# Kernel optimization log

Hardware: AMD Instinct MI355X
Metric: run time of the kernel (lower is better)

Reference implementation:

```python
import jax, jax.numpy as jnp
import numpy as np

B, S, E, C = 128, 256, 768, 4


def setup_inputs() -> dict:
    key = jax.random.key(0)
    ks = jax.random.split(key, 8)
    questions = jax.random.normal(ks[0], (B, E), dtype=jnp.float32)
    segments = jax.random.normal(ks[1], (B, S, E), dtype=jnp.float32)
    W1 = jax.random.normal(ks[2], (2 * E, E), dtype=jnp.float32) * 0.02
    b1 = jnp.zeros((E,), dtype=jnp.float32)
    W2 = jax.random.normal(ks[3], (E, E // 2), dtype=jnp.float32) * 0.02
    b2 = jnp.zeros((E // 2,), dtype=jnp.float32)
    W3 = jax.random.normal(ks[4], (E // 2, C), dtype=jnp.float32) * 0.02
    b3 = jnp.zeros((C,), dtype=jnp.float32)
    num_segments = jax.random.randint(ks[5], (B,), 1, S + 1, dtype=jnp.int32)
    return {"questions": questions, "segments": segments, "W1": W1, "b1": b1,
            "W2": W2, "b2": b2, "W3": W3, "b3": b3, "num_segments": num_segments}


def reference(questions, segments, W1, b1, W2, b2, W3, b3, num_segments):
    # --- MLP instance scores (call()): concat question emb with every segment emb ---
    q = jnp.broadcast_to(questions[:, None, :], segments.shape)      # [B,S,E]
    x = jnp.concatenate([q, segments], axis=-1)                      # [B,S,2E]
    h = jax.nn.gelu(x @ W1 + b1, approximate=False)                  # keras gelu is exact
    h = jax.nn.gelu(h @ W2 + b2, approximate=False)
    preds = jax.nn.softmax(h @ W3 + b3, axis=-1)                     # [B,S,C]

    # --- per-bag noisy-OR style aggregation (aggregate_loss inner math, vectorized) ---
    # In the TF code, for class cid: s_j = sum(preds[j,:cid]) (exclusive cumsum over
    # classes), and product_of_sum_prob ACCUMULATES across the i loop, so
    # update_i = preds[i,cid] * cumprod_i( prod_{j!=k} s_j ) (leave-one-out products).
    mask = jnp.arange(S)[None, :] < num_segments[:, None]            # [B,S]
    mC = mask[..., None]                                             # [B,S,1]
    s = jnp.cumsum(preds, axis=-1) - preds                           # exclusive cumsum, [B,S,C]
    s_m = jnp.where(mC, s, 1.0)                                      # padded -> multiplicative identity
    # leave-one-out product over the segment axis via prefix/suffix cumprods
    cp_f = jnp.cumprod(s_m, axis=1)
    prefix = jnp.concatenate([jnp.ones_like(s_m[:, :1]), cp_f[:, :-1]], axis=1)
    cp_b = jnp.cumprod(s_m[:, ::-1], axis=1)[:, ::-1]
    suffix = jnp.concatenate([cp_b[:, 1:], jnp.ones_like(s_m[:, :1])], axis=1)
    L = prefix * suffix                                              # prod_{j!=k} s_j, [B,S,C]
    cpL = jnp.cumprod(L, axis=1)                                     # running product over i (padding is at the end)
    sum_term = jnp.sum(jnp.where(mC, preds * cpL, 0.0), axis=1)      # [B,C]
    prod_term = jnp.prod(jnp.where(mC, preds, 1.0), axis=1)          # prod_i preds[i,cid]
    agg = sum_term / jnp.float32(C) + prod_term                      # bag_pred_agg_scores, [B,C]
    return agg
```

## Files before the change

kernel.cpp:

```cpp
#include <hip/hip_runtime.h>
#include <hip/hip_bf16.h>


typedef __attribute__((ext_vector_type(8))) short short8;
typedef __attribute__((ext_vector_type(8))) unsigned short ushort8;
typedef __attribute__((ext_vector_type(16))) float f32x16;
typedef __attribute__((ext_vector_type(8))) int i32x8;
typedef __attribute__((ext_vector_type(4))) int i32x4;

__device__ __forceinline__ unsigned short f2bf(float f) {
    union { float f; unsigned int u; } c; c.f = f;
    unsigned int u = c.u;
    unsigned int r = (u + 0x7FFFu + ((u >> 16) & 1u)) >> 16;
    return (unsigned short)r;
}
__device__ __forceinline__ float bf2f(unsigned short u) {
    union { unsigned int u; float f; } c; c.u = ((unsigned int)u) << 16;
    return c.f;
}
__device__ __forceinline__ float gelu_fast(float x) {
    float x2 = x * x;
    float y2 = 1.5957691216057308f * (x + 0.044715f * x2 * x);
    float e = __expf(y2);
    float t = 1.0f - 2.0f * __builtin_amdgcn_rcpf(e + 1.0f);
    return 0.5f * x * (1.0f + t);
}

typedef const __attribute__((address_space(1))) void* gas_t;
typedef __attribute__((address_space(3))) void* las_t;
__device__ __forceinline__ void g2l16(const void* g, void* l) {
    __builtin_amdgcn_global_load_lds((gas_t)g, (las_t)l, 16, 0, 0);
}

__device__ __forceinline__ unsigned int f4_to_fp8x4(float a, float b, float c, float d) {
    int lo = __builtin_amdgcn_cvt_pk_fp8_f32(a, b, 0, 0);
    return (unsigned int)__builtin_amdgcn_cvt_pk_fp8_f32(c, d, lo, 1);
}
__device__ __forceinline__ unsigned char f_to_fp8(float a) {
    return (unsigned char)(__builtin_amdgcn_cvt_pk_fp8_f32(a, a, 0, 0) & 0xFF);
}

#define PREP_Q    96
#define PREP_TR1E 240
#define PREP_TR2E 312
#define PREP_END  12600

__global__ __launch_bounds__(256) void prep_kernel(
    const float* __restrict__ segments, unsigned char* __restrict__ segF8,
    const float* __restrict__ W1, unsigned char* __restrict__ W1t8,
    const float* __restrict__ W2, unsigned char* __restrict__ W2t8,
    const float* __restrict__ questions, float* __restrict__ qW1p)
{
    __shared__ __align__(16) char sh[16640];
    const int bid = blockIdx.x, tid = threadIdx.x;

    if (bid < PREP_Q) {
        const int s = bid / 24, rem = bid % 24;
        const int n0 = (rem % 12) * 64, m0 = (rem / 12) * 64;
        float (*As)[64] = (float(*)[64])sh;
        float (*Bs)[64] = (float(*)[64])(sh + 4096);
        const int tn = tid & 15, tm = tid >> 4;
        float acc[4][4] = {};
        const int la_m = tid >> 2;
        const int la_k = (tid & 3) << 2;
        const int lb_k = tid >> 4;
        const int lb_n = (tid & 15) << 2;
        const float* Aptr = questions + (size_t)(m0 + la_m) * 768 + la_k;
        const float* Bptr = W1 + (size_t)lb_k * 768 + n0 + lb_n;
        const int kbeg = s * 192, kend = kbeg + 192;
        for (int k0 = kbeg; k0 < kend; k0 += 16) {
            float4 av = *(const float4*)(Aptr + k0);
            float4 bv = *(const float4*)(Bptr + (size_t)k0 * 768);
            As[la_k + 0][la_m] = av.x;
            As[la_k + 1][la_m] = av.y;
            As[la_k + 2][la_m] = av.z;
            As[la_k + 3][la_m] = av.w;
            *(float4*)&Bs[lb_k][lb_n] = bv;
            __syncthreads();
            #pragma unroll
            for (int k = 0; k < 16; k++) {
                float4 a = *(const float4*)&As[k][tm << 2];
                float4 b = *(const float4*)&Bs[k][tn << 2];
                float ar[4] = {a.x, a.y, a.z, a.w};
                float br[4] = {b.x, b.y, b.z, b.w};
                #pragma unroll
                for (int i = 0; i < 4; i++)
                    #pragma unroll
                    for (int j = 0; j < 4; j++)
                        acc[i][j] += ar[i] * br[j];
            }
            __syncthreads();
        }
        float* outp = qW1p + (size_t)s * 128 * 768;
        #pragma unroll
        for (int i = 0; i < 4; i++) {
            int row = m0 + (tm << 2) + i;
            int colBase = n0 + (tn << 2);
            *(float4*)&outp[(size_t)row * 768 + colBase] =
                make_float4(acc[i][0], acc[i][1], acc[i][2], acc[i][3]);
        }
        return;
    }

    if (bid < PREP_TR2E) {
        const float* in; unsigned char* outp; int R, C, bx, by;
        if (bid < PREP_TR1E) {
            int idx = bid - PREP_Q; bx = idx % 12; by = idx / 12;
            in = W1 + 768 * 768; outp = W1t8; R = 768; C = 768;
        } else {
            int idx = bid - PREP_TR1E; bx = idx % 6; by = idx / 6;
            in = W2; outp = W2t8; R = 768; C = 384;
        }
        float (*t)[65] = (float(*)[65])sh;
        int r0 = by * 64, c0 = bx * 64;
        int tx = tid & 63, ty = tid >> 6;
        #pragma unroll
        for (int p = 0; p < 16; p++) {
            int row = ty * 16 + p;
            t[row][tx] = in[(size_t)(r0 + row) * C + c0 + tx];
        }
        __syncthreads();
        #pragma unroll
        for (int p = 0; p < 16; p++) {
            int orow = ty * 16 + p;
            outp[(size_t)(c0 + orow) * R + r0 + tx] = f_to_fp8(t[tx][orow]);
        }
        return;
    }

    {
        long i = (long)(bid - PREP_TR2E) * 256 + tid;
        const float4* in = (const float4*)segments;
        float4 a = in[2 * i], b = in[2 * i + 1];
        unsigned int lo = f4_to_fp8x4(a.x, a.y, a.z, a.w);
        unsigned int hi = f4_to_fp8x4(b.x, b.y, b.z, b.w);
        *(uint2*)(segF8 + i * 8) = make_uint2(lo, hi);
    }
}

template<int MODE>
__global__ __launch_bounds__(256) void mfma_gemm_f8(
    const unsigned char* __restrict__ A8,
    const unsigned char* __restrict__ Bt8,
    const float* __restrict__ bias,
    const float* __restrict__ rowAdd,
    void* __restrict__ CoutV,
    int M, int N, int K,
    const float* __restrict__ W3p)
{
    __shared__ __align__(16) unsigned char smem8[32768 + (MODE == 2 ? 2048 : 0)];
    unsigned char* As = smem8;
    unsigned char* Bs = smem8 + 8192;
    const int tid = threadIdx.x;
    const int wave = tid >> 6, lane = tid & 63;
    const int m0 = blockIdx.y * 128, n0 = blockIdx.x * 128;
    const int wm = (wave & 1) * 64, wn = (wave >> 1) * 64;

    if constexpr (MODE == 2) {
        if (tid < 128)
            ((float4*)(smem8 + 32768))[tid] = ((const float4*)W3p)[n0 + tid];
    }

    f32x16 acc[2][2] = {};

    const int srow = tid >> 2;
    const int schunk = (tid & 3) ^ ((srow >> 1) & 3);
    const unsigned char* Ag = A8 + (size_t)(m0 + srow) * K + schunk * 16;
    const unsigned char* Bg = Bt8 + (size_t)(n0 + srow) * K + schunk * 16;
    unsigned char* Al = As + tid * 16;
    unsigned char* Bl = Bs + tid * 16;

    const int fm = lane & 31, fq = lane >> 5;

    for (int k0 = 0; k0 < K; k0 += 64) {
        g2l16(Ag + k0, Al);
        g2l16(Ag + (size_t)64 * K + k0, Al + 4096);
        g2l16(Bg + k0, Bl);
        g2l16(Bg + (size_t)64 * K + k0, Bl + 4096);
        __syncthreads();

        i32x8 av[2], bv[2];
        #pragma unroll
        for (int i = 0; i < 2; i++) {
            int rw = wm + i * 32 + fm, key = (rw >> 1) & 3;
            i32x4 lo = *(const i32x4*)&As[rw * 64 + (((fq << 1) | 0) ^ key) * 16];
            i32x4 hi = *(const i32x4*)&As[rw * 64 + (((fq << 1) | 1) ^ key) * 16];
            av[i][0] = lo[0]; av[i][1] = lo[1]; av[i][2] = lo[2]; av[i][3] = lo[3];
            av[i][4] = hi[0]; av[i][5] = hi[1]; av[i][6] = hi[2]; av[i][7] = hi[3];
        }
        #pragma unroll
        for (int j = 0; j < 2; j++) {
            int rw = wn + j * 32 + fm, key = (rw >> 1) & 3;
            i32x4 lo = *(const i32x4*)&Bs[rw * 64 + (((fq << 1) | 0) ^ key) * 16];
            i32x4 hi = *(const i32x4*)&Bs[rw * 64 + (((fq << 1) | 1) ^ key) * 16];
            bv[j][0] = lo[0]; bv[j][1] = lo[1]; bv[j][2] = lo[2]; bv[j][3] = lo[3];
            bv[j][4] = hi[0]; bv[j][5] = hi[1]; bv[j][6] = hi[2]; bv[j][7] = hi[3];
        }
        #pragma unroll
        for (int i = 0; i < 2; i++)
            #pragma unroll
            for (int j = 0; j < 2; j++)
                acc[i][j] = __builtin_amdgcn_mfma_scale_f32_32x32x64_f8f6f4(
                    av[i], bv[j], acc[i][j], 0, 0,
                    0, 127, 0, 127);
        __syncthreads();
    }

    #pragma unroll
    for (int j = 0; j < 2; j++) {
        int coll = wn + j * 32 + fm;
        int col = n0 + coll;
        float add = bias[col];
        if (rowAdd) {
            const float* radd = rowAdd + (size_t)(m0 >> 8) * N;
            add += radd[col] + radd[col + 98304] +
                   radd[col + 2 * 98304] + radd[col + 3 * 98304];
        }
        #pragma unroll
        for (int i = 0; i < 2; i++) {
            int rbase = wm + i * 32 + 4 * fq;
            #pragma unroll
            for (int reg = 0; reg < 16; reg++) {
                int rowl = rbase + (reg & 3) + 8 * (reg >> 2);
                float v = gelu_fast(acc[i][j][reg] + add);
                if constexpr (MODE == 1) smem8[rowl * 128 + coll] = f_to_fp8(v);
                else ((unsigned short*)smem8)[rowl * 128 + coll] = f2bf(v);
            }
        }
    }
    __syncthreads();
    if constexpr (MODE == 1) {
        unsigned char* Cout = (unsigned char*)CoutV;
        #pragma unroll
        for (int it = 0; it < 4; it++) {
            int idx = it * 256 + tid;
            int r = idx >> 3, cc = (idx & 7) * 16;
            *(uint4*)&Cout[(size_t)(m0 + r) * N + n0 + cc] =
                *(const uint4*)&smem8[r * 128 + cc];
        }
    } else if constexpr (MODE == 2) {
        const float4* w3sh = (const float4*)(smem8 + 32768);
        const unsigned short* tile = (const unsigned short*)smem8;
        int r = tid >> 1, ch = tid & 1;
        const unsigned short* rowp = tile + r * 128 + ch * 64;
        float4 a = make_float4(0.f, 0.f, 0.f, 0.f);
        #pragma unroll
        for (int k = 0; k < 8; k++) {
            int kk = k ^ (r & 7);
            ushort8 u = *(const ushort8*)(rowp + kk * 8);
            #pragma unroll
            for (int jj = 0; jj < 8; jj++) {
                float h = bf2f(u[jj]);
                float4 wv2 = w3sh[ch * 64 + kk * 8 + jj];
                a.x += h * wv2.x; a.y += h * wv2.y;
                a.z += h * wv2.z; a.w += h * wv2.w;
            }
        }
        a.x += __shfl_xor(a.x, 1); a.y += __shfl_xor(a.y, 1);
        a.z += __shfl_xor(a.z, 1); a.w += __shfl_xor(a.w, 1);
        if (ch == 0)
            ((float4*)CoutV)[(size_t)blockIdx.x * 32768 + m0 + r] = a;
    } else {
        unsigned short* Cout = (unsigned short*)CoutV;
        #pragma unroll
        for (int it = 0; it < 8; it++) {
            int idx = it * 256 + tid;
            int r = idx >> 4, cc = (idx & 15) * 8;
            *(ushort8*)&Cout[(size_t)(m0 + r) * N + n0 + cc] =
                *(const ushort8*)&((unsigned short*)smem8)[r * 128 + cc];
        }
    }
}

__device__ __forceinline__ float4 f4mul(float4 a, float4 b) {
    return make_float4(a.x * b.x, a.y * b.y, a.z * b.z, a.w * b.w);
}

__device__ __forceinline__ float4 block_scan_prod(float4 v, int lane, int wv,
                                                  float4* wtot) {
    #pragma unroll
    for (int off = 1; off < 64; off <<= 1) {
        float4 t;
        t.x = __shfl_up(v.x, off); t.y = __shfl_up(v.y, off);
        t.z = __shfl_up(v.z, off); t.w = __shfl_up(v.w, off);
        if (lane >= off) v = f4mul(v, t);
    }
    if (lane == 63) wtot[wv] = v;
    __syncthreads();
    float4 pre = make_float4(1.f, 1.f, 1.f, 1.f);
    #pragma unroll
    for (int w = 0; w < 3; w++)
        if (w < wv) pre = f4mul(pre, wtot[w]);
    __syncthreads();
    return f4mul(pre, v);
}

__global__ __launch_bounds__(256) void head_kernel(
    const float* __restrict__ pp,
    const float* __restrict__ b3,
    const int* __restrict__ nseg,
    float* __restrict__ out)
{
    __shared__ float4 xbuf[256];
    __shared__ float4 wtot[4];
    const int b = blockIdx.x, tid = threadIdx.x;
    const int lane = tid & 63, wv = tid >> 6;
    const float4 ones = make_float4(1.f, 1.f, 1.f, 1.f);

    const float4* ppv = (const float4*)pp;
    size_t row = (size_t)b * 256 + tid;
    float4 a0 = ppv[row], a1 = ppv[row + 32768], a2 = ppv[row + 65536];
    float4 acc = make_float4(a0.x + a1.x + a2.x + b3[0],
                             a0.y + a1.y + a2.y + b3[1],
                             a0.z + a1.z + a2.z + b3[2],
                             a0.w + a1.w + a2.w + b3[3]);
    float m = fmaxf(fmaxf(acc.x, acc.y), fmaxf(acc.z, acc.w));
    float e0 = __expf(acc.x - m), e1 = __expf(acc.y - m),
          e2 = __expf(acc.z - m), e3 = __expf(acc.w - m);
    float inv = 1.0f / (e0 + e1 + e2 + e3);
    float4 p = make_float4(e0 * inv, e1 * inv, e2 * inv, e3 * inv);

    const int n = nseg[b];
    bool msk = tid < n;
    float s1 = p.x, s2 = s1 + p.y, s3 = s2 + p.z;
    float4 sm = msk ? make_float4(0.f, s1, s2, s3) : ones;

    float4 isc = block_scan_prod(sm, lane, wv, wtot);
    xbuf[tid] = isc;
    __syncthreads();
    float4 pfx = (tid > 0) ? xbuf[tid - 1] : ones;
    __syncthreads();

    xbuf[255 - tid] = sm;
    __syncthreads();
    float4 rsm = xbuf[tid];
    __syncthreads();
    float4 risc = block_scan_prod(rsm, lane, wv, wtot);
    xbuf[tid] = risc;
    __syncthreads();
    float4 sfx = (tid < 255) ? xbuf[254 - tid] : ones;
    __syncthreads();

    float4 L = f4mul(pfx, sfx);
    float4 cpL = block_scan_prod(L, lane, wv, wtot);

    float4 term = msk ? f4mul(p, cpL) : make_float4(0.f, 0.f, 0.f, 0.f);
    float4 pm = msk ? p : ones;
    #pragma unroll
    for (int off = 32; off > 0; off >>= 1) {
        term.x += __shfl_xor(term.x, off); term.y += __shfl_xor(term.y, off);
        term.z += __shfl_xor(term.z, off); term.w += __shfl_xor(term.w, off);
        pm.x *= __shfl_xor(pm.x, off); pm.y *= __shfl_xor(pm.y, off);
        pm.z *= __shfl_xor(pm.z, off); pm.w *= __shfl_xor(pm.w, off);
    }
    if (lane == 0) { xbuf[wv] = term; xbuf[4 + wv] = pm; }
    __syncthreads();
    if (tid == 0) {
        float4 st = make_float4(0.f, 0.f, 0.f, 0.f);
        float4 pr = ones;
        #pragma unroll
        for (int w = 0; w < 4; w++) {
            float4 t = xbuf[w], q = xbuf[4 + w];
            st.x += t.x; st.y += t.y; st.z += t.z; st.w += t.w;
            pr = f4mul(pr, q);
        }
        ((float4*)out)[b] = make_float4(0.25f * st.x + pr.x,
                                        0.25f * st.y + pr.y,
                                        0.25f * st.z + pr.z,
                                        0.25f * st.w + pr.w);
    }
}

extern "C" void kernel_launch(void* const* d_in, const int* in_sizes, int n_in,
                              void* d_out, int out_size, void* d_ws, size_t ws_size,
                              hipStream_t stream) {
    (void)in_sizes; (void)n_in; (void)out_size; (void)ws_size;
    const float* questions = (const float*)d_in[0];
    const float* segments  = (const float*)d_in[1];
    const float* W1 = (const float*)d_in[2];
    const float* b1 = (const float*)d_in[3];
    const float* W2 = (const float*)d_in[4];
    const float* b2 = (const float*)d_in[5];
    const float* W3 = (const float*)d_in[6];
    const float* b3 = (const float*)d_in[7];
    const int*  nseg = (const int*)d_in[8];
    float* out = (float*)d_out;

    char* w = (char*)d_ws;
    float* qW1p = (float*)w;                   w += (size_t)4 * 128 * 768 * 4;
    unsigned char*  W1t8 = (unsigned char*)w;  w += (size_t)768 * 768;
    unsigned char*  W2t8 = (unsigned char*)w;  w += (size_t)384 * 768;
    unsigned char*  segF8 = (unsigned char*)w; w += (size_t)32768 * 768;
    unsigned char*  H1f8 = (unsigned char*)w;  w += (size_t)32768 * 768;
    float* ppreds = (float*)w;                 w += (size_t)3 * 32768 * 4 * 4;

    prep_kernel<<<PREP_END, 256, 0, stream>>>(
        segments, segF8, W1, W1t8, W2, W2t8, questions, qW1p);
    mfma_gemm_f8<1><<<dim3(6, 256), 256, 0, stream>>>(
        segF8, W1t8, b1, qW1p, H1f8, 32768, 768, 768, nullptr);
    mfma_gemm_f8<2><<<dim3(3, 256), 256, 0, stream>>>(
        H1f8, W2t8, b2, nullptr, ppreds, 32768, 384, 768, W3);
    head_kernel<<<128, 256, 0, stream>>>(ppreds, b3, nseg, out);
}
```

Before: 243.9 us.

## Double-buffer GEMM K loop, swizzle block order, and split question projection kernel

The fp8 MFMA GEMM now double-buffers its LDS tiles, issuing the next K-slab's global-to-LDS loads before computing on the current one, and drops one barrier per iteration. Block indices are remapped in an XCD-aware swizzle so neighbouring tiles share L2. The question×W1 projection moves into its own kernel that uses 8 K-splits with larger per-thread tiles and no per-step syncs, and the GEMM epilogue sums 8 partials instead of 4. The aim is to hide load latency and improve cache locality, at the cost of an extra kernel launch and more partial-sum reads.

```diff
diff --git a/kernel.cpp b/kernel.cpp
--- a/kernel.cpp
+++ b/kernel.cpp
@@ -40,75 +40,73 @@
     return (unsigned char)(__builtin_amdgcn_cvt_pk_fp8_f32(a, a, 0, 0) & 0xFF);
 }
 
-#define PREP_Q    96
-#define PREP_TR1E 240
-#define PREP_TR2E 312
-#define PREP_END  12600
-
-__global__ __launch_bounds__(256) void prep_kernel(
+__global__ __launch_bounds__(256) void prep_q_kernel(
+    const float* __restrict__ questions, const float* __restrict__ W1,
+    float* __restrict__ qW1p)
+{
+    __shared__ __align__(16) float As[96][132];
+    __shared__ __align__(16) float Bs[96][64];
+    const int tid = threadIdx.x;
+    const int nt = blockIdx.x % 12, sp = blockIdx.x / 12;
+    const int n0 = nt * 64, kbeg = sp * 96;
+
+    for (int i = tid; i < 3072; i += 256) {
+        int row = i / 24, c4 = i % 24;
+        float4 v = ((const float4*)questions)[row * 192 + (kbeg >> 2) + c4];
+        int kb = c4 * 4;
+        As[kb + 0][row] = v.x; As[kb + 1][row] = v.y;
+        As[kb + 2][row] = v.z; As[kb + 3][row] = v.w;
+    }
+    for (int i = tid; i < 1536; i += 256) {
+        int row = i / 16, c4 = i % 16;
+        float4 v = ((const float4*)W1)[(size_t)(kbeg + row) * 192 + (n0 >> 2) + c4];
+        *(float4*)&Bs[row][c4 * 4] = v;
+    }
+    __syncthreads();
+
+    const int tm = tid >> 4, tn = tid & 15;
+    float acc[8][4] = {};
+    #pragma unroll 2
+    for (int k = 0; k < 96; k++) {
+        float4 a0 = *(const float4*)&As[k][tm * 8];
+        float4 a1 = *(const float4*)&As[k][tm * 8 + 4];
+        float4 b  = *(const float4*)&Bs[k][tn * 4];
+        float ar[8] = {a0.x, a0.y, a0.z, a0.w, a1.x, a1.y, a1.z, a1.w};
+        float br[4] = {b.x, b.y, b.z, b.w};
+        #pragma unroll
+        for (int i = 0; i < 8; i++)
+            #pragma unroll
+            for (int j = 0; j < 4; j++)
+                acc[i][j] += ar[i] * br[j];
+    }
+    float* outp = qW1p + (size_t)sp * 128 * 768;
+    #pragma unroll
+    for (int i = 0; i < 8; i++) {
+        int row = tm * 8 + i;
+        *(float4*)&outp[(size_t)row * 768 + n0 + tn * 4] =
+            make_float4(acc[i][0], acc[i][1], acc[i][2], acc[i][3]);
+    }
+}
+
+#define PR_TR1E 144
+#define PR_TR2E 216
+#define PR_END  12504
+
+__global__ __launch_bounds__(256) void prep_rest_kernel(
     const float* __restrict__ segments, unsigned char* __restrict__ segF8,
     const float* __restrict__ W1, unsigned char* __restrict__ W1t8,
-    const float* __restrict__ W2, unsigned char* __restrict__ W2t8,
-    const float* __restrict__ questions, float* __restrict__ qW1p)
+    const float* __restrict__ W2, unsigned char* __restrict__ W2t8)
 {
     __shared__ __align__(16) char sh[16640];
     const int bid = blockIdx.x, tid = threadIdx.x;
 
-    if (bid < PREP_Q) {
-        const int s = bid / 24, rem = bid % 24;
-        const int n0 = (rem % 12) * 64, m0 = (rem / 12) * 64;
-        float (*As)[64] = (float(*)[64])sh;
-        float (*Bs)[64] = (float(*)[64])(sh + 4096);
-        const int tn = tid & 15, tm = tid >> 4;
-        float acc[4][4] = {};
-        const int la_m = tid >> 2;
-        const int la_k = (tid & 3) << 2;
-        const int lb_k = tid >> 4;
-        const int lb_n = (tid & 15) << 2;
-        const float* Aptr = questions + (size_t)(m0 + la_m) * 768 + la_k;
-        const float* Bptr = W1 + (size_t)lb_k * 768 + n0 + lb_n;
-        const int kbeg = s * 192, kend = kbeg + 192;
-        for (int k0 = kbeg; k0 < kend; k0 += 16) {
-            float4 av = *(const float4*)(Aptr + k0);
-            float4 bv = *(const float4*)(Bptr + (size_t)k0 * 768);
-            As[la_k + 0][la_m] = av.x;
-            As[la_k + 1][la_m] = av.y;
-            As[la_k + 2][la_m] = av.z;
-            As[la_k + 3][la_m] = av.w;
-            *(float4*)&Bs[lb_k][lb_n] = bv;
-            __syncthreads();
-            #pragma unroll
-            for (int k = 0; k < 16; k++) {
-                float4 a = *(const float4*)&As[k][tm << 2];
-                float4 b = *(const float4*)&Bs[k][tn << 2];
-                float ar[4] = {a.x, a.y, a.z, a.w};
-                float br[4] = {b.x, b.y, b.z, b.w};
-                #pragma unroll
-                for (int i = 0; i < 4; i++)
-                    #pragma unroll
-                    for (int j = 0; j < 4; j++)
-                        acc[i][j] += ar[i] * br[j];
-            }
-            __syncthreads();
-        }
-        float* outp = qW1p + (size_t)s * 128 * 768;
-        #pragma unroll
-        for (int i = 0; i < 4; i++) {
-            int row = m0 + (tm << 2) + i;
-            int colBase = n0 + (tn << 2);
-            *(float4*)&outp[(size_t)row * 768 + colBase] =
-                make_float4(acc[i][0], acc[i][1], acc[i][2], acc[i][3]);
-        }
-        return;
-    }
-
-    if (bid < PREP_TR2E) {
+    if (bid < PR_TR2E) {
         const float* in; unsigned char* outp; int R, C, bx, by;
-        if (bid < PREP_TR1E) {
-            int idx = bid - PREP_Q; bx = idx % 12; by = idx / 12;
+        if (bid < PR_TR1E) {
+            int idx = bid; bx = idx % 12; by = idx / 12;
             in = W1 + 768 * 768; outp = W1t8; R = 768; C = 768;
         } else {
-            int idx = bid - PREP_TR1E; bx = idx % 6; by = idx / 6;
+            int idx = bid - PR_TR1E; bx = idx % 6; by = idx / 6;
             in = W2; outp = W2t8; R = 768; C = 384;
         }
         float (*t)[65] = (float(*)[65])sh;
@@ -129,7 +127,7 @@
     }
 
     {
-        long i = (long)(bid - PREP_TR2E) * 256 + tid;
+        long i = (long)(bid - PR_TR2E) * 256 + tid;
         const float4* in = (const float4*)segments;
         float4 a = in[2 * i], b = in[2 * i + 1];
         unsigned int lo = f4_to_fp8x4(a.x, a.y, a.z, a.w);
@@ -149,11 +147,14 @@
     const float* __restrict__ W3p)
 {
     __shared__ __align__(16) unsigned char smem8[32768 + (MODE == 2 ? 2048 : 0)];
-    unsigned char* As = smem8;
-    unsigned char* Bs = smem8 + 8192;
     const int tid = threadIdx.x;
     const int wave = tid >> 6, lane = tid & 63;
-    const int m0 = blockIdx.y * 128, n0 = blockIdx.x * 128;
+
+    const int nwg = gridDim.x * gridDim.y;
+    const int bidl = blockIdx.y * gridDim.x + blockIdx.x;
+    const int cpx = nwg >> 3;
+    const int swz = (bidl & 7) * cpx + (bidl >> 3);
+    const int m0 = (swz / gridDim.x) * 128, n0 = (swz % gridDim.x) * 128;
     const int wm = (wave & 1) * 64, wn = (wave >> 1) * 64;
 
     if constexpr (MODE == 2) {
@@ -167,18 +168,25 @@
     const int schunk = (tid & 3) ^ ((srow >> 1) & 3);
     const unsigned char* Ag = A8 + (size_t)(m0 + srow) * K + schunk * 16;
     const unsigned char* Bg = Bt8 + (size_t)(n0 + srow) * K + schunk * 16;
-    unsigned char* Al = As + tid * 16;
-    unsigned char* Bl = Bs + tid * 16;
 
     const int fm = lane & 31, fq = lane >> 5;
 
+#define STAGE_K(buf, kk) do {                                   \
+        unsigned char* _d = smem8 + (buf) * 16384 + tid * 16;   \
+        g2l16(Ag + (kk), _d);                                   \
+        g2l16(Ag + (size_t)64 * K + (kk), _d + 4096);           \
+        g2l16(Bg + (kk), _d + 8192);                            \
+        g2l16(Bg + (size_t)64 * K + (kk), _d + 12288);          \
+    } while (0)
+
+    STAGE_K(0, 0);
+    __syncthreads();
+    int cur = 0;
     for (int k0 = 0; k0 < K; k0 += 64) {
-        g2l16(Ag + k0, Al);
-        g2l16(Ag + (size_t)64 * K + k0, Al + 4096);
-        g2l16(Bg + k0, Bl);
-        g2l16(Bg + (size_t)64 * K + k0, Bl + 4096);
-        __syncthreads();
-
+        if (k0 + 64 < K) STAGE_K(cur ^ 1, k0 + 64);
+
+        const unsigned char* As = smem8 + cur * 16384;
+        const unsigned char* Bs = As + 8192;
         i32x8 av[2], bv[2];
         #pragma unroll
         for (int i = 0; i < 2; i++) {
@@ -204,7 +212,9 @@
                     av[i], bv[j], acc[i][j], 0, 0,
                     0, 127, 0, 127);
         __syncthreads();
-    }
+        cur ^= 1;
+    }
+#undef STAGE_K
 
     #pragma unroll
     for (int j = 0; j < 2; j++) {
@@ -212,9 +222,9 @@
         int col = n0 + coll;
         float add = bias[col];
         if (rowAdd) {
-            const float* radd = rowAdd + (size_t)(m0 >> 8) * N;
-            add += radd[col] + radd[col + 98304] +
-                   radd[col + 2 * 98304] + radd[col + 3 * 98304];
+            const float* radd = rowAdd + (size_t)(m0 >> 8) * N + col;
+            #pragma unroll
+            for (int s = 0; s < 8; s++) add += radd[(size_t)s * 98304];
         }
         #pragma unroll
         for (int i = 0; i < 2; i++) {
@@ -259,16 +269,7 @@
         a.x += __shfl_xor(a.x, 1); a.y += __shfl_xor(a.y, 1);
         a.z += __shfl_xor(a.z, 1); a.w += __shfl_xor(a.w, 1);
         if (ch == 0)
-            ((float4*)CoutV)[(size_t)blockIdx.x * 32768 + m0 + r] = a;
-    } else {
-        unsigned short* Cout = (unsigned short*)CoutV;
-        #pragma unroll
-        for (int it = 0; it < 8; it++) {
-            int idx = it * 256 + tid;
-            int r = idx >> 4, cc = (idx & 15) * 8;
-            *(ushort8*)&Cout[(size_t)(m0 + r) * N + n0 + cc] =
-                *(const ushort8*)&((unsigned short*)smem8)[r * 128 + cc];
-        }
+            ((float4*)CoutV)[(size_t)(n0 >> 7) * 32768 + m0 + r] = a;
     }
 }
 
@@ -387,15 +388,16 @@
     float* out = (float*)d_out;
 
     char* w = (char*)d_ws;
-    float* qW1p = (float*)w;                   w += (size_t)4 * 128 * 768 * 4;
+    float* qW1p = (float*)w;                   w += (size_t)8 * 128 * 768 * 4;
     unsigned char*  W1t8 = (unsigned char*)w;  w += (size_t)768 * 768;
     unsigned char*  W2t8 = (unsigned char*)w;  w += (size_t)384 * 768;
     unsigned char*  segF8 = (unsigned char*)w; w += (size_t)32768 * 768;
     unsigned char*  H1f8 = (unsigned char*)w;  w += (size_t)32768 * 768;
     float* ppreds = (float*)w;                 w += (size_t)3 * 32768 * 4 * 4;
 
-    prep_kernel<<<PREP_END, 256, 0, stream>>>(
-        segments, segF8, W1, W1t8, W2, W2t8, questions, qW1p);
+    prep_rest_kernel<<<PR_END, 256, 0, stream>>>(
+        segments, segF8, W1, W1t8, W2, W2t8);
+    prep_q_kernel<<<96, 256, 0, stream>>>(questions, W1, qW1p);
     mfma_gemm_f8<1><<<dim3(6, 256), 256, 0, stream>>>(
         segF8, W1t8, b1, qW1p, H1f8, 32768, 768, 768, nullptr);
     mfma_gemm_f8<2><<<dim3(3, 256), 256, 0, stream>>>(
```

After: 253.1 us. 1.04x slower.
